# Performance work log

Hardware: AMD Instinct MI355X
Metric: run time of the kernel (lower is better)

The kernel has to match this reference:

```python
import jax, jax.numpy as jnp
import numpy as np
from jax import lax

EPS = 1e-5

def _odconv(x, W, fc_w, bn_g, bn_b, ch_w, ch_b, fl_w, fl_b, sp_w, sp_b, kn_w, kn_b):
    # x: [B,Cin,H,W]; W: [K,Cout,Cin,ks,ks] (kernel_num K candidate kernels)
    B = x.shape[0]
    K, Cout, Cin, ks, _ = W.shape
    pooled = jnp.mean(x, (2, 3))                          # global avg pool -> [B,Cin]
    h = pooled @ fc_w.T                                   # 1x1 conv (no bias) -> [B,A]
    m = jnp.mean(h, 0)
    v = jnp.var(h, 0)
    h = jax.nn.relu((h - m) * lax.rsqrt(v + EPS) * bn_g + bn_b)  # BN (train mode, batch stats)
    ch_att = jax.nn.sigmoid(h @ ch_w.T + ch_b)            # channel attention [B,Cin]
    fl_att = jax.nn.sigmoid(h @ fl_w.T + fl_b)            # filter attention  [B,Cout]
    sp_att = jax.nn.sigmoid(h @ sp_w.T + sp_b).reshape(B, 1, 1, 1, ks, ks)   # spatial
    kn_att = jax.nn.softmax(h @ kn_w.T + kn_b, axis=1).reshape(B, K, 1, 1, 1, 1)  # kernel
    # per-sample aggregated kernel: sum_k kn_att*sp_att*W -> [B,Cout,Cin,ks,ks]
    agg_w = jnp.sum(kn_att * sp_att * W[None], axis=1)
    xw = x * ch_att[:, :, None, None]
    pad = (ks - 1) // 2
    def conv1(xi, wi):  # per-sample conv == batch-as-groups trick in torch
        return lax.conv_general_dilated(xi[None], wi, (1, 1), [(pad, pad), (pad, pad)],
                                        dimension_numbers=('NCHW', 'OIHW', 'NCHW'))[0]
    out = jax.vmap(conv1)(xw, agg_w)                      # [B,Cout,H,W]
    return out * fl_att[:, :, None, None]

def _bn_relu(x, g, b):
    m = jnp.mean(x, (0, 2, 3), keepdims=True)
    v = jnp.var(x, (0, 2, 3), keepdims=True)
    return jax.nn.relu((x - m) * lax.rsqrt(v + EPS) * g.reshape(1, -1, 1, 1) + b.reshape(1, -1, 1, 1))

def setup_inputs() -> dict:
    key = jax.random.key(0)
    B, Cin, Cout, H, Wd = 16, 64, 128, 128, 128
    K, ks, A = 4, 3, 16  # kernel_num, kernel_size, attention_channel=max(int(C*0.0625),16)
    ks_ = [jax.random.fold_in(key, i) for i in range(32)]
    n = lambda k, shp, s=0.05: jax.random.normal(k, shp, jnp.float32) * s
    d = {'x': jax.random.normal(ks_[0], (B, Cin, H, Wd), jnp.float32)}
    # layer 1 (Cin->Cout)
    d.update(w1=n(ks_[1], (K, Cout, Cin, ks, ks)),
             a_fc_w=n(ks_[2], (A, Cin)), a_bn_g=jnp.ones(A), a_bn_b=jnp.zeros(A),
             a_ch_w=n(ks_[3], (Cin, A)), a_ch_b=jnp.zeros(Cin),
             a_fl_w=n(ks_[4], (Cout, A)), a_fl_b=jnp.zeros(Cout),
             a_sp_w=n(ks_[5], (ks * ks, A)), a_sp_b=jnp.zeros(ks * ks),
             a_kn_w=n(ks_[6], (K, A)), a_kn_b=jnp.zeros(K),
             bn1_g=jnp.ones(Cout), bn1_b=jnp.zeros(Cout))
    # layer 2 (Cout->Cout)
    d.update(w2=n(ks_[7], (K, Cout, Cout, ks, ks)),
             b_fc_w=n(ks_[8], (A, Cout)), b_bn_g=jnp.ones(A), b_bn_b=jnp.zeros(A),
             b_ch_w=n(ks_[9], (Cout, A)), b_ch_b=jnp.zeros(Cout),
             b_fl_w=n(ks_[10], (Cout, A)), b_fl_b=jnp.zeros(Cout),
             b_sp_w=n(ks_[11], (ks * ks, A)), b_sp_b=jnp.zeros(ks * ks),
             b_kn_w=n(ks_[12], (K, A)), b_kn_b=jnp.zeros(K),
             bn2_g=jnp.ones(Cout), bn2_b=jnp.zeros(Cout))
    return d

def reference(x, w1, a_fc_w, a_bn_g, a_bn_b, a_ch_w, a_ch_b, a_fl_w, a_fl_b,
              a_sp_w, a_sp_b, a_kn_w, a_kn_b, bn1_g, bn1_b,
              w2, b_fc_w, b_bn_g, b_bn_b, b_ch_w, b_ch_b, b_fl_w, b_fl_b,
              b_sp_w, b_sp_b, b_kn_w, b_kn_b, bn2_g, bn2_b):
    h = _odconv(x, w1, a_fc_w, a_bn_g, a_bn_b, a_ch_w, a_ch_b, a_fl_w, a_fl_b,
                a_sp_w, a_sp_b, a_kn_w, a_kn_b)
    h = _bn_relu(h, bn1_g, bn1_b)
    h = _odconv(h, w2, b_fc_w, b_bn_g, b_bn_b, b_ch_w, b_ch_b, b_fl_w, b_fl_b,
                b_sp_w, b_sp_b, b_kn_w, b_kn_b)
    return _bn_relu(h, bn2_g, bn2_b)
```

## Files before the change

### kernel.cpp

```cpp
#include <hip/hip_runtime.h>
#include <hip/hip_bf16.h>
#include <math.h>

#define EPS 1e-5f

typedef __attribute__((ext_vector_type(8))) short bf16x8;
typedef __attribute__((ext_vector_type(4))) float f32x4;

__device__ inline ushort f2bf(float f) {
    uint u = __float_as_uint(f);
    uint r = (u + 0x7fffu + ((u >> 16) & 1u)) >> 16;
    return (ushort)r;
}
__device__ inline float bf2f(ushort u) {
    return __uint_as_float(((uint)u) << 16);
}
__device__ inline float sigmoidf_(float x) { return 1.f / (1.f + expf(-x)); }

__device__ inline void gload16(const void* g, void* l) {
    __builtin_amdgcn_global_load_lds((const __attribute__((address_space(1))) unsigned int*)g,
                                     (__attribute__((address_space(3))) unsigned int*)l,
                                     16, 0, 0);
}

__global__ void attn_kernel(const float* __restrict__ pooled,
                            const float* __restrict__ fc_w,
                            const float* __restrict__ bn_g, const float* __restrict__ bn_b,
                            const float* __restrict__ ch_w, const float* __restrict__ ch_b,
                            const float* __restrict__ fl_w, const float* __restrict__ fl_b,
                            const float* __restrict__ sp_w, const float* __restrict__ sp_b,
                            const float* __restrict__ kn_w, const float* __restrict__ kn_b,
                            float* __restrict__ ch_att, float* __restrict__ fl_att,
                            float* __restrict__ sp_att, float* __restrict__ kn_att,
                            int C, int Cout) {
    const int Bb = 16, A = 16, K = 4;
    __shared__ float h[16][16];
    int tid = threadIdx.x;

    if (tid < Bb * A) {
        int b = tid >> 4, a = tid & 15;
        const float* pr = pooled + b * C;
        const float* fw = fc_w + a * C;
        float s = 0.f;
        for (int c = 0; c < C; c++) s += pr[c] * fw[c];
        h[b][a] = s;
    }
    __syncthreads();

    if (tid < A) {
        int a = tid;
        float m = 0.f;
        for (int b = 0; b < Bb; b++) m += h[b][a];
        m *= (1.f / 16.f);
        float v = 0.f;
        for (int b = 0; b < Bb; b++) { float d = h[b][a] - m; v += d * d; }
        v *= (1.f / 16.f);
        float inv = rsqrtf(v + EPS);
        float g = bn_g[a], bb = bn_b[a];
        for (int b = 0; b < Bb; b++) {
            float t = (h[b][a] - m) * inv * g + bb;
            h[b][a] = t > 0.f ? t : 0.f;
        }
    }
    __syncthreads();

    for (int idx = tid; idx < Bb * C; idx += blockDim.x) {
        int b = idx / C, c = idx % C;
        float s = ch_b[c];
        #pragma unroll
        for (int a = 0; a < A; a++) s += h[b][a] * ch_w[c * A + a];
        ch_att[idx] = sigmoidf_(s);
    }
    for (int idx = tid; idx < Bb * Cout; idx += blockDim.x) {
        int b = idx / Cout, o = idx % Cout;
        float s = fl_b[o];
        #pragma unroll
        for (int a = 0; a < A; a++) s += h[b][a] * fl_w[o * A + a];
        fl_att[idx] = sigmoidf_(s);
    }
    for (int idx = tid; idx < Bb * 9; idx += blockDim.x) {
        int b = idx / 9, r = idx % 9;
        float s = sp_b[r];
        #pragma unroll
        for (int a = 0; a < A; a++) s += h[b][a] * sp_w[r * A + a];
        sp_att[idx] = sigmoidf_(s);
    }
    if (tid < Bb) {
        int b = tid;
        float l[K], mx = -1e30f;
        #pragma unroll
        for (int k = 0; k < K; k++) {
            float s = kn_b[k];
            #pragma unroll
            for (int a = 0; a < A; a++) s += h[b][a] * kn_w[k * A + a];
            l[k] = s; mx = fmaxf(mx, s);
        }
        float den = 0.f;
        #pragma unroll
        for (int k = 0; k < K; k++) { l[k] = expf(l[k] - mx); den += l[k]; }
        #pragma unroll
        for (int k = 0; k < K; k++) kn_att[b * K + k] = l[k] / den;
    }
}

__global__ void waggF_kernel(const float* __restrict__ W4, const float* __restrict__ ch,
                             const float* __restrict__ fl, const float* __restrict__ sp,
                             const float* __restrict__ kn, ushort* __restrict__ WbF,
                             int Cout, int Cin, int NT, int N) {
    int idx = blockIdx.x * blockDim.x + threadIdx.x;
    if (idx >= N) return;
    int e = idx & 7;
    int l = (idx >> 3) & 63;
    int ot = (idx >> 9) & 7;
    int tb = idx >> 12;
    int t = tb % NT, b = tb / NT;
    int o = ot * 16 + (l & 15);
    int k = t * 32 + ((l >> 4) << 3) + e;
    int rs = k / Cin, i = k - rs * Cin;
    size_t kstride = (size_t)Cout * Cin * 9;
    const float* wp = W4 + ((size_t)o * Cin + i) * 9 + rs;
    const float* kp = kn + b * 4;
    float s = kp[0] * wp[0] + kp[1] * wp[kstride] + kp[2] * wp[2 * kstride] + kp[3] * wp[3 * kstride];
    float v = fl[b * Cout + o] * ch[b * Cin + i] * sp[b * 9 + rs] * s;
    WbF[idx] = f2bf(v);
}

__global__ __launch_bounds__(256) void trans_kernel(const float* __restrict__ in32,
                                                    const ushort* __restrict__ in16,
                                                    ushort* __restrict__ out,
                                                    float* __restrict__ ppart,
                                                    const float* __restrict__ stats,
                                                    const float* __restrict__ g,
                                                    const float* __restrict__ beta,
                                                    int C, int doBN) {
    int tilesC = C >> 5;
    int cbi = blockIdx.x % tilesC;
    int pbi = blockIdx.x / tilesC;
    int cb = cbi << 5, pb = pbi << 5;
    int y = blockIdx.y, b = blockIdx.z;
    __shared__ float tile[32][33];
    int t = threadIdx.x;
    int p = t & 31, c0 = t >> 5;
    float vj[4];
    #pragma unroll
    for (int j = 0; j < 4; j++) {
        int cl = c0 + j * 8;
        int c = cb + cl;
        size_t idx = (((size_t)b * C + c) * 128 + y) * 128 + pb + p;
        float v = in16 ? bf2f(in16[idx]) : in32[idx];
        if (doBN) {
            v = (v - stats[2 * c]) * stats[2 * c + 1] * g[c] + beta[c];
            v = fmaxf(v, 0.f);
        }
        tile[cl][p] = v;
        vj[j] = v;
    }
    #pragma unroll
    for (int j = 0; j < 4; j++) {
        float s = vj[j];
        #pragma unroll
        for (int msk = 1; msk < 32; msk <<= 1) s += __shfl_xor(s, msk);
        if (p == 0) {
            int cl = c0 + j * 8;
            ppart[((size_t)((b * tilesC + cbi) * 32 + cl)) * 512 + pbi * 128 + y] = s;
        }
    }
    __syncthreads();
    int c2 = (t & 15) << 1, pp = t >> 4;
    #pragma unroll
    for (int j = 0; j < 2; j++) {
        int p2 = pp + j * 16;
        uint lo = f2bf(tile[c2][p2]);
        uint hi = f2bf(tile[c2 + 1][p2]);
        *(uint*)&out[(((size_t)b * 128 + y) * 128 + pb + p2) * C + cb + c2] = lo | (hi << 16);
    }
}

__global__ void poolred_kernel(const float* __restrict__ part, float* __restrict__ pool) {
    int bc = blockIdx.x;
    const float* p = part + (size_t)bc * 512;
    float s = 0.f;
    for (int i = threadIdx.x; i < 512; i += 128) s += p[i];
    #pragma unroll
    for (int off = 32; off; off >>= 1) s += __shfl_down(s, off);
    __shared__ float tmp[2];
    if ((threadIdx.x & 63) == 0) tmp[threadIdx.x >> 6] = s;
    __syncthreads();
    if (!threadIdx.x) pool[bc] = (tmp[0] + tmp[1]) * (1.f / 16384.f);
}

__global__ __launch_bounds__(256, 3) void conv_mfma(const ushort* __restrict__ xT,
                                                    const ushort* __restrict__ WbF,
                                                    float* __restrict__ outF,
                                                    ushort* __restrict__ out16,
                                                    float* __restrict__ part,
                                                    int Cin, int use16) {
    const int BUFSH = 3 * 130 * 32;
    __shared__ short sx[2 * BUFSH];
    __shared__ float sred[4][64][2];
    int id = blockIdx.x;
    int swz = (id & 7) * (gridDim.x >> 3) + (id >> 3);
    int y = swz & 127, b = swz >> 7;
    int tid = threadIdx.x;
    int lane = tid & 63, wid = tid >> 6;
    int wm = wid >> 1, wn = wid & 1;
    int Cdiv32 = Cin >> 5;
    int NC = Cdiv32;
    int NT = 9 * Cdiv32;

    f32x4 acc[4][4] = {};

    {
        bf16x8 z = {};
        for (int e = tid * 8; e < 2 * BUFSH; e += 2048) *(bf16x8*)&sx[e] = z;
    }
    __syncthreads();

    const size_t rowstride = (size_t)128 * Cin;

    auto stage = [&](int bi, int ck) {
        #pragma unroll
        for (int j = 0; j < 6; j++) {
            int cc = wid + 4 * j;
            int r = cc >> 3, q = cc & 7;
            int yy = y + r - 1;
            if ((unsigned)yy < 128u) {
                int u = (q << 6) + lane;
                int P = (u >> 2) + 1;
                int slog = (u & 3) ^ ((P >> 1) & 3);
                const ushort* gp = xT + (size_t)(b * 128 + yy) * rowstride
                                      + (size_t)(P - 1) * Cin + (ck << 5) + (slog << 3);
                short* lp = &sx[bi * BUFSH + (r * 130 + 1) * 32 + (q << 9)];
                gload16(gp, lp);
            }
        }
    };

    stage(0, 0);
    __syncthreads();

    const bf16x8* Ab = (const bf16x8*)WbF;
    size_t abase = (size_t)b * NT;

    for (int ck = 0; ck < NC; ck++) {
        if (ck + 1 < NC) stage((ck + 1) & 1, ck + 1);
        const short* bb = &sx[(ck & 1) * BUFSH];
        #pragma unroll
        for (int rs = 0; rs < 9; rs++) {
            int rr = (rs / 3) * 130;
            int dx = rs % 3 - 1;
            int t = rs * Cdiv32 + ck;
            bf16x8 a[4], bv[4];
            size_t ai = ((abase + t) * 8 + wm * 4) * 64 + lane;
            #pragma unroll
            for (int m = 0; m < 4; m++) a[m] = Ab[ai + (size_t)m * 64];
            int Pb = wn * 64 + (lane & 15) + dx + 1;
            int slog = lane >> 4;
            #pragma unroll
            for (int n = 0; n < 4; n++) {
                int P = Pb + n * 16;
                bv[n] = *(const bf16x8*)&bb[(rr + P) * 32 + ((slog ^ ((P >> 1) & 3)) << 3)];
            }
            #pragma unroll
            for (int m = 0; m < 4; m++)
                #pragma unroll
                for (int n = 0; n < 4; n++)
                    acc[m][n] = __builtin_amdgcn_mfma_f32_16x16x32_bf16(
                        a[m], bv[n], acc[m][n], 0, 0, 0);
        }
        __syncthreads();
    }

    int px = wn * 64 + (lane & 15);
    int orow0 = wm * 64 + ((lane >> 4) << 2);
    if (use16) {
        #pragma unroll
        for (int m = 0; m < 4; m++)
            #pragma unroll
            for (int r = 0; r < 4; r++) {
                int oc = orow0 + m * 16 + r;
                ushort* po = out16 + ((size_t)(b * 128 + oc) * 128 + y) * 128 + px;
                #pragma unroll
                for (int n = 0; n < 4; n++) po[n * 16] = f2bf(acc[m][n][r]);
            }
    } else {
        #pragma unroll
        for (int m = 0; m < 4; m++)
            #pragma unroll
            for (int r = 0; r < 4; r++) {
                int oc = orow0 + m * 16 + r;
                float* po = outF + ((size_t)(b * 128 + oc) * 128 + y) * 128 + px;
                #pragma unroll
                for (int n = 0; n < 4; n++) po[n * 16] = acc[m][n][r];
            }
    }

    #pragma unroll
    for (int m = 0; m < 4; m++)
        #pragma unroll
        for (int r = 0; r < 4; r++) {
            float s = 0.f, q = 0.f;
            #pragma unroll
            for (int n = 0; n < 4; n++) { float v = acc[m][n][r]; s += v; q += v * v; }
            #pragma unroll
            for (int msk = 1; msk < 16; msk <<= 1) {
                s += __shfl_xor(s, msk);
                q += __shfl_xor(q, msk);
            }
            if ((lane & 15) == 0) {
                int chl = m * 16 + ((lane >> 4) << 2) + r;
                sred[wid][chl][0] = s;
                sred[wid][chl][1] = q;
            }
        }
    __syncthreads();
    {
        int ch = tid >> 1, v = tid & 1;
        int wmc = ch >> 6, chl = ch & 63;
        float t2 = sred[wmc * 2][chl][v] + sred[wmc * 2 + 1][chl][v];
        part[((size_t)(b * 128 + y)) * 256 + tid] = t2;
    }
}

__global__ void bnred_kernel(const float* __restrict__ part, float* __restrict__ stats) {
    int c = blockIdx.x;
    float s = 0.f, q = 0.f;
    for (int by = threadIdx.x; by < 2048; by += blockDim.x) {
        s += part[(size_t)by * 256 + 2 * c];
        q += part[(size_t)by * 256 + 2 * c + 1];
    }
    #pragma unroll
    for (int off = 32; off; off >>= 1) { s += __shfl_down(s, off); q += __shfl_down(q, off); }
    __shared__ float ss[4], qq[4];
    int lane = threadIdx.x & 63, w = threadIdx.x >> 6;
    if (!lane) { ss[w] = s; qq[w] = q; }
    __syncthreads();
    if (!threadIdx.x) {
        s = ss[0] + ss[1] + ss[2] + ss[3];
        q = qq[0] + qq[1] + qq[2] + qq[3];
        const float n = 16.f * 16384.f;
        float m = s / n;
        float var = q / n - m * m;
        stats[2 * c] = m;
        stats[2 * c + 1] = rsqrtf(var + EPS);
    }
}

__global__ void bnapply_kernel(float4* __restrict__ buf, const float* __restrict__ stats,
                               const float* __restrict__ g, const float* __restrict__ bta,
                               size_t N4) {
    size_t idx = (size_t)blockIdx.x * blockDim.x + threadIdx.x;
    size_t stride = (size_t)gridDim.x * blockDim.x;
    for (; idx < N4; idx += stride) {
        int c = (int)((idx >> 12) & 127);
        float sc = stats[2 * c + 1] * g[c];
        float sh = bta[c] - stats[2 * c] * sc;
        float4 v = buf[idx];
        v.x = fmaxf(v.x * sc + sh, 0.f);
        v.y = fmaxf(v.y * sc + sh, 0.f);
        v.z = fmaxf(v.z * sc + sh, 0.f);
        v.w = fmaxf(v.w * sc + sh, 0.f);
        buf[idx] = v;
    }
}

__global__ void bnapply16_kernel(const ushort* __restrict__ in, float4* __restrict__ out,
                                 const float* __restrict__ stats,
                                 const float* __restrict__ g, const float* __restrict__ bta,
                                 size_t N4) {
    size_t idx = (size_t)blockIdx.x * blockDim.x + threadIdx.x;
    size_t stride = (size_t)gridDim.x * blockDim.x;
    for (; idx < N4; idx += stride) {
        int c = (int)((idx >> 12) & 127);
        float sc = stats[2 * c + 1] * g[c];
        float sh = bta[c] - stats[2 * c] * sc;
        ushort4 u = *(const ushort4*)&in[idx * 4];
        float4 v;
        v.x = fmaxf(bf2f(u.x) * sc + sh, 0.f);
        v.y = fmaxf(bf2f(u.y) * sc + sh, 0.f);
        v.z = fmaxf(bf2f(u.z) * sc + sh, 0.f);
        v.w = fmaxf(bf2f(u.w) * sc + sh, 0.f);
        out[idx] = v;
    }
}

extern "C" void kernel_launch(void* const* d_in, const int* in_sizes, int n_in,
                              void* d_out, int out_size, void* d_ws, size_t ws_size,
                              hipStream_t stream) {
    const int B = 16, Cin1 = 64, C = 128, H = 128, W = 128, HW = H * W;

    const float* x      = (const float*)d_in[0];
    const float* w1     = (const float*)d_in[1];
    const float* a_fc_w = (const float*)d_in[2];
    const float* a_bn_g = (const float*)d_in[3];
    const float* a_bn_b = (const float*)d_in[4];
    const float* a_ch_w = (const float*)d_in[5];
    const float* a_ch_b = (const float*)d_in[6];
    const float* a_fl_w = (const float*)d_in[7];
    const float* a_fl_b = (const float*)d_in[8];
    const float* a_sp_w = (const float*)d_in[9];
    const float* a_sp_b = (const float*)d_in[10];
    const float* a_kn_w = (const float*)d_in[11];
    const float* a_kn_b = (const float*)d_in[12];
    const float* bn1_g  = (const float*)d_in[13];
    const float* bn1_b  = (const float*)d_in[14];
    const float* w2     = (const float*)d_in[15];
    const float* b_fc_w = (const float*)d_in[16];
    const float* b_bn_g = (const float*)d_in[17];
    const float* b_bn_b = (const float*)d_in[18];
    const float* b_ch_w = (const float*)d_in[19];
    const float* b_ch_b = (const float*)d_in[20];
    const float* b_fl_w = (const float*)d_in[21];
    const float* b_fl_b = (const float*)d_in[22];
    const float* b_sp_w = (const float*)d_in[23];
    const float* b_sp_b = (const float*)d_in[24];
    const float* b_kn_w = (const float*)d_in[25];
    const float* b_kn_b = (const float*)d_in[26];
    const float* bn2_g  = (const float*)d_in[27];
    const float* bn2_b  = (const float*)d_in[28];

    float* out = (float*)d_out;
    float* ws  = (float*)d_ws;

    float* XTf   = ws;
    ushort* xT   = (ushort*)XTf;
    float* WBf   = XTf + 16777216;
    ushort* WbF  = (ushort*)WBf;
    float* CPART = WBf + 1179648;
    float* PPART = CPART + 524288;
    float* POOL  = PPART + 1048576;
    float* CH    = POOL + 2048;
    float* FL    = CH + 2048;
    float* SP    = FL + 2048;
    float* KN    = SP + 160;
    float* ST    = KN + 64;
    float* XH2f  = ST + 256;
    ushort* xhat2 = (ushort*)XH2f;

    size_t need = ((size_t)(XH2f - ws) + 16777216) * sizeof(float);
    int fit2 = ws_size >= need;

    ushort* xhat1 = (ushort*)out;

    trans_kernel<<<dim3((Cin1 / 32) * 4, H, B), 256, 0, stream>>>(
        x, nullptr, xT, PPART, ST, nullptr, nullptr, Cin1, 0);
    poolred_kernel<<<B * Cin1, 128, 0, stream>>>(PPART, POOL);
    attn_kernel<<<1, 256, 0, stream>>>(POOL, a_fc_w, a_bn_g, a_bn_b, a_ch_w, a_ch_b,
                                       a_fl_w, a_fl_b, a_sp_w, a_sp_b, a_kn_w, a_kn_b,
                                       CH, FL, SP, KN, Cin1, C);
    int NT1 = 9 * Cin1 / 32;
    int N1 = B * NT1 * 4096;
    waggF_kernel<<<(N1 + 255) / 256, 256, 0, stream>>>(w1, CH, FL, SP, KN, WbF, C, Cin1, NT1, N1);
    conv_mfma<<<H * B, 256, 0, stream>>>(xT, WbF, nullptr, xhat1, CPART, Cin1, 1);
    bnred_kernel<<<C, 256, 0, stream>>>(CPART, ST);
    trans_kernel<<<dim3((C / 32) * 4, H, B), 256, 0, stream>>>(
        nullptr, xhat1, xT, PPART, ST, bn1_g, bn1_b, C, 1);

    poolred_kernel<<<B * C, 128, 0, stream>>>(PPART, POOL);
    attn_kernel<<<1, 256, 0, stream>>>(POOL, b_fc_w, b_bn_g, b_bn_b, b_ch_w, b_ch_b,
                                       b_fl_w, b_fl_b, b_sp_w, b_sp_b, b_kn_w, b_kn_b,
                                       CH, FL, SP, KN, C, C);
    int NT2 = 9 * C / 32;
    int N2 = B * NT2 * 4096;
    waggF_kernel<<<(N2 + 255) / 256, 256, 0, stream>>>(w2, CH, FL, SP, KN, WbF, C, C, NT2, N2);
    if (fit2) {
        conv_mfma<<<H * B, 256, 0, stream>>>(xT, WbF, nullptr, xhat2, CPART, C, 1);
        bnred_kernel<<<C, 256, 0, stream>>>(CPART, ST);
        bnapply16_kernel<<<2048, 256, 0, stream>>>(xhat2, (float4*)out, ST, bn2_g, bn2_b,
                                                   (size_t)B * C * HW / 4);
    } else {
        conv_mfma<<<H * B, 256, 0, stream>>>(xT, WbF, out, nullptr, CPART, C, 0);
        bnred_kernel<<<C, 256, 0, stream>>>(CPART, ST);
        bnapply_kernel<<<2048, 256, 0, stream>>>((float4*)out, ST, bn2_g, bn2_b,
                                                 (size_t)B * C * HW / 4);
    }
}
```

Measured before the change: 377.9 us.

## Compute two output rows per conv block to reuse staged input halo rows

The MFMA conv block now covers two output rows using 512 threads (8 waves), staging 4 input rows instead of 3 per row, so halo rows are shared between the two outputs. Per-output-row global/LDS staging traffic drops and weight (A) fragments are loaded per wave as before. The BN partial-sum reduction is restructured across 4 column/row waves, and bnred takes the new row count. LDS use grows and occupancy drops to 2 blocks of 512 threads, and the grid halves.

Measured after the change: 430.0 us. 1.14x slower.

```diff
diff --git a/kernel.cpp b/kernel.cpp
--- a/kernel.cpp
+++ b/kernel.cpp
@@ -189,21 +189,24 @@
     if (!threadIdx.x) pool[bc] = (tmp[0] + tmp[1]) * (1.f / 16384.f);
 }
 
-__global__ __launch_bounds__(256, 3) void conv_mfma(const ushort* __restrict__ xT,
+__global__ __launch_bounds__(512, 2) void conv_mfma(const ushort* __restrict__ xT,
                                                     const ushort* __restrict__ WbF,
                                                     float* __restrict__ outF,
                                                     ushort* __restrict__ out16,
                                                     float* __restrict__ part,
                                                     int Cin, int use16) {
-    const int BUFSH = 3 * 130 * 32;
+    const int BUFSH = 4 * 130 * 32;
     __shared__ short sx[2 * BUFSH];
-    __shared__ float sred[4][64][2];
+    __shared__ float sred[8][64][2];
     int id = blockIdx.x;
     int swz = (id & 7) * (gridDim.x >> 3) + (id >> 3);
-    int y = swz & 127, b = swz >> 7;
+    int yp = swz & 63, b = swz >> 6;
+    int y0 = yp << 1;
     int tid = threadIdx.x;
     int lane = tid & 63, wid = tid >> 6;
-    int wm = wid >> 1, wn = wid & 1;
+    int wm = wid >> 2;
+    int wn = wid & 3;
+    int wnrow = wn >> 1, wncol = wn & 1;
     int Cdiv32 = Cin >> 5;
     int NC = Cdiv32;
     int NT = 9 * Cdiv32;
@@ -212,7 +215,7 @@
 
     {
         bf16x8 z = {};
-        for (int e = tid * 8; e < 2 * BUFSH; e += 2048) *(bf16x8*)&sx[e] = z;
+        for (int e = tid * 8; e < 2 * BUFSH; e += 4096) *(bf16x8*)&sx[e] = z;
     }
     __syncthreads();
 
@@ -220,10 +223,10 @@
 
     auto stage = [&](int bi, int ck) {
         #pragma unroll
-        for (int j = 0; j < 6; j++) {
-            int cc = wid + 4 * j;
+        for (int j = 0; j < 4; j++) {
+            int cc = wid + 8 * j;
             int r = cc >> 3, q = cc & 7;
-            int yy = y + r - 1;
+            int yy = y0 + r - 1;
             if ((unsigned)yy < 128u) {
                 int u = (q << 6) + lane;
                 int P = (u >> 2) + 1;
@@ -247,19 +250,19 @@
         const short* bb = &sx[(ck & 1) * BUFSH];
         #pragma unroll
         for (int rs = 0; rs < 9; rs++) {
-            int rr = (rs / 3) * 130;
+            int rowL = wnrow + rs / 3;
             int dx = rs % 3 - 1;
             int t = rs * Cdiv32 + ck;
             bf16x8 a[4], bv[4];
             size_t ai = ((abase + t) * 8 + wm * 4) * 64 + lane;
             #pragma unroll
             for (int m = 0; m < 4; m++) a[m] = Ab[ai + (size_t)m * 64];
-            int Pb = wn * 64 + (lane & 15) + dx + 1;
+            int Pb = wncol * 64 + (lane & 15) + dx + 1;
             int slog = lane >> 4;
             #pragma unroll
             for (int n = 0; n < 4; n++) {
                 int P = Pb + n * 16;
-                bv[n] = *(const bf16x8*)&bb[(rr + P) * 32 + ((slog ^ ((P >> 1) & 3)) << 3)];
+                bv[n] = *(const bf16x8*)&bb[(rowL * 130 + P) * 32 + ((slog ^ ((P >> 1) & 3)) << 3)];
             }
             #pragma unroll
             for (int m = 0; m < 4; m++)
@@ -271,7 +274,8 @@
         __syncthreads();
     }
 
-    int px = wn * 64 + (lane & 15);
+    int y = y0 + wnrow;
+    int px = wncol * 64 + (lane & 15);
     int orow0 = wm * 64 + ((lane >> 4) << 2);
     if (use16) {
         #pragma unroll
@@ -309,23 +313,48 @@
             }
             if ((lane & 15) == 0) {
                 int chl = m * 16 + ((lane >> 4) << 2) + r;
-                sred[wid][chl][0] = s;
-                sred[wid][chl][1] = q;
+                if (wn == 0) { sred[wid][chl][0] = s; sred[wid][chl][1] = q; }
             }
         }
     __syncthreads();
-    {
+    #pragma unroll
+    for (int w2 = 1; w2 < 4; w2++) {
+        if (wn == w2) {
+            #pragma unroll
+            for (int m = 0; m < 4; m++)
+                #pragma unroll
+                for (int r = 0; r < 4; r++) {
+                    float s = 0.f, q = 0.f;
+                    #pragma unroll
+                    for (int n = 0; n < 4; n++) { float v = acc[m][n][r]; s += v; q += v * v; }
+                    #pragma unroll
+                    for (int msk = 1; msk < 16; msk <<= 1) {
+                        s += __shfl_xor(s, msk);
+                        q += __shfl_xor(q, msk);
+                    }
+                    if ((lane & 15) == 0) {
+                        int chl = m * 16 + ((lane >> 4) << 2) + r;
+                        sred[wm * 4 + w2][chl][0] = s;
+                        sred[wm * 4 + w2][chl][1] = q;
+                    }
+                }
+        }
+    }
+    __syncthreads();
+    if (tid < 256) {
         int ch = tid >> 1, v = tid & 1;
         int wmc = ch >> 6, chl = ch & 63;
-        float t2 = sred[wmc * 2][chl][v] + sred[wmc * 2 + 1][chl][v];
-        part[((size_t)(b * 128 + y)) * 256 + tid] = t2;
-    }
-}
-
-__global__ void bnred_kernel(const float* __restrict__ part, float* __restrict__ stats) {
+        float t2 = sred[wmc * 4 + 0][chl][v] + sred[wmc * 4 + 1][chl][v]
+                 + sred[wmc * 4 + 2][chl][v] + sred[wmc * 4 + 3][chl][v];
+        part[((size_t)(b * 64 + yp)) * 256 + tid] = t2;
+    }
+}
+
+__global__ void bnred_kernel(const float* __restrict__ part, float* __restrict__ stats,
+                             int nrows) {
     int c = blockIdx.x;
     float s = 0.f, q = 0.f;
-    for (int by = threadIdx.x; by < 2048; by += blockDim.x) {
+    for (int by = threadIdx.x; by < nrows; by += blockDim.x) {
         s += part[(size_t)by * 256 + 2 * c];
         q += part[(size_t)by * 256 + 2 * c + 1];
     }
@@ -451,8 +480,8 @@
     int NT1 = 9 * Cin1 / 32;
     int N1 = B * NT1 * 4096;
     waggF_kernel<<<(N1 + 255) / 256, 256, 0, stream>>>(w1, CH, FL, SP, KN, WbF, C, Cin1, NT1, N1);
-    conv_mfma<<<H * B, 256, 0, stream>>>(xT, WbF, nullptr, xhat1, CPART, Cin1, 1);
-    bnred_kernel<<<C, 256, 0, stream>>>(CPART, ST);
+    conv_mfma<<<H * B / 2, 512, 0, stream>>>(xT, WbF, nullptr, xhat1, CPART, Cin1, 1);
+    bnred_kernel<<<C, 256, 0, stream>>>(CPART, ST, 1024);
     trans_kernel<<<dim3((C / 32) * 4, H, B), 256, 0, stream>>>(
         nullptr, xhat1, xT, PPART, ST, bn1_g, bn1_b, C, 1);
 
@@ -464,13 +493,13 @@
     int N2 = B * NT2 * 4096;
     waggF_kernel<<<(N2 + 255) / 256, 256, 0, stream>>>(w2, CH, FL, SP, KN, WbF, C, C, NT2, N2);
     if (fit2) {
-        conv_mfma<<<H * B, 256, 0, stream>>>(xT, WbF, nullptr, xhat2, CPART, C, 1);
-        bnred_kernel<<<C, 256, 0, stream>>>(CPART, ST);
+        conv_mfma<<<H * B / 2, 512, 0, stream>>>(xT, WbF, nullptr, xhat2, CPART, C, 1);
+        bnred_kernel<<<C, 256, 0, stream>>>(CPART, ST, 1024);
         bnapply16_kernel<<<2048, 256, 0, stream>>>(xhat2, (float4*)out, ST, bn2_g, bn2_b,
                                                    (size_t)B * C * HW / 4);
     } else {
-        conv_mfma<<<H * B, 256, 0, stream>>>(xT, WbF, out, nullptr, CPART, C, 0);
-        bnred_kernel<<<C, 256, 0, stream>>>(CPART, ST);
+        conv_mfma<<<H * B / 2, 512, 0, stream>>>(xT, WbF, out, nullptr, CPART, C, 0);
+        bnred_kernel<<<C, 256, 0, stream>>>(CPART, ST, 1024);
         bnapply_kernel<<<2048, 256, 0, stream>>>((float4*)out, ST, bn2_g, bn2_b,
                                                  (size_t)B * C * HW / 4);
     }
```

## Switch conv to 32x32x16 MFMA with register-prefetched weights and templated Cin

Applied to the files above, without the earlier changes.

Replaces the 16x16x32 bf16 MFMA tiling with 32x32x16 MFMA fragments and re-lays out the aggregated weight buffer in 32-row by 16-k tiles to match. Weight fragments are now double-buffered in registers, with the next step's loads issued ahead of the current MFMAs. Cin becomes a template parameter so the loop over channel chunks and taps fully unrolls. The goals are fewer MFMA and LDS instructions per FLOP and hiding global weight-load latency, at the cost of more register pressure and a reworked epilogue and reduction mapping.

After: 417.5 us. 10.5% more time.

```diff
diff --git a/kernel.cpp b/kernel.cpp
--- a/kernel.cpp
+++ b/kernel.cpp
@@ -6,6 +6,7 @@
 
 typedef __attribute__((ext_vector_type(8))) short bf16x8;
 typedef __attribute__((ext_vector_type(4))) float f32x4;
+typedef __attribute__((ext_vector_type(16))) float f32x16;
 
 __device__ inline ushort f2bf(float f) {
     uint u = __float_as_uint(f);
@@ -106,17 +107,17 @@
 __global__ void waggF_kernel(const float* __restrict__ W4, const float* __restrict__ ch,
                              const float* __restrict__ fl, const float* __restrict__ sp,
                              const float* __restrict__ kn, ushort* __restrict__ WbF,
-                             int Cout, int Cin, int NT, int N) {
+                             int Cout, int Cin, int NK16, int NKT, int N) {
     int idx = blockIdx.x * blockDim.x + threadIdx.x;
     if (idx >= N) return;
     int e = idx & 7;
     int l = (idx >> 3) & 63;
-    int ot = (idx >> 9) & 7;
-    int tb = idx >> 12;
-    int t = tb % NT, b = tb / NT;
-    int o = ot * 16 + (l & 15);
-    int k = t * 32 + ((l >> 4) << 3) + e;
-    int rs = k / Cin, i = k - rs * Cin;
+    int ot = (idx >> 9) & 3;
+    int tb = idx >> 11;
+    int kt = tb % NKT, b = tb / NKT;
+    int o = (ot << 5) + (l & 31);
+    int rs = kt / NK16, i16 = kt - rs * NK16;
+    int i = (i16 << 4) + ((l >> 5) << 3) + e;
     size_t kstride = (size_t)Cout * Cin * 9;
     const float* wp = W4 + ((size_t)o * Cin + i) * 9 + rs;
     const float* kp = kn + b * 4;
@@ -189,26 +190,27 @@
     if (!threadIdx.x) pool[bc] = (tmp[0] + tmp[1]) * (1.f / 16384.f);
 }
 
+template<int CIN>
 __global__ __launch_bounds__(256, 3) void conv_mfma(const ushort* __restrict__ xT,
                                                     const ushort* __restrict__ WbF,
                                                     float* __restrict__ outF,
                                                     ushort* __restrict__ out16,
                                                     float* __restrict__ part,
-                                                    int Cin, int use16) {
+                                                    int use16) {
     const int BUFSH = 3 * 130 * 32;
     __shared__ short sx[2 * BUFSH];
     __shared__ float sred[4][64][2];
+    const int NK16 = CIN >> 4;
+    const int NC = CIN >> 5;
+    const int NKT = 9 * NK16;
     int id = blockIdx.x;
     int swz = (id & 7) * (gridDim.x >> 3) + (id >> 3);
     int y = swz & 127, b = swz >> 7;
     int tid = threadIdx.x;
     int lane = tid & 63, wid = tid >> 6;
     int wm = wid >> 1, wn = wid & 1;
-    int Cdiv32 = Cin >> 5;
-    int NC = Cdiv32;
-    int NT = 9 * Cdiv32;
-
-    f32x4 acc[4][4] = {};
+
+    f32x16 acc[2][2] = {};
 
     {
         bf16x8 z = {};
@@ -216,7 +218,7 @@
     }
     __syncthreads();
 
-    const size_t rowstride = (size_t)128 * Cin;
+    const size_t rowstride = (size_t)128 * CIN;
 
     auto stage = [&](int bi, int ck) {
         #pragma unroll
@@ -229,7 +231,7 @@
                 int P = (u >> 2) + 1;
                 int slog = (u & 3) ^ ((P >> 1) & 3);
                 const ushort* gp = xT + (size_t)(b * 128 + yy) * rowstride
-                                      + (size_t)(P - 1) * Cin + (ck << 5) + (slog << 3);
+                                      + (size_t)(P - 1) * CIN + (ck << 5) + (slog << 3);
                 short* lp = &sx[bi * BUFSH + (r * 130 + 1) * 32 + (q << 9)];
                 gload16(gp, lp);
             }
@@ -237,78 +239,90 @@
     };
 
     stage(0, 0);
-    __syncthreads();
 
     const bf16x8* Ab = (const bf16x8*)WbF;
-    size_t abase = (size_t)b * NT;
-
-    for (int ck = 0; ck < NC; ck++) {
-        if (ck + 1 < NC) stage((ck + 1) & 1, ck + 1);
+    const size_t abase = (size_t)b * NKT;
+
+    bf16x8 aR[2][2][2];
+    #pragma unroll
+    for (int kt2 = 0; kt2 < 2; kt2++)
+        #pragma unroll
+        for (int mf = 0; mf < 2; mf++)
+            aR[0][kt2][mf] = Ab[((abase + kt2) * 4 + (wm * 2 + mf)) * 64 + lane];
+
+    __syncthreads();
+
+    int pxb = wn * 64 + (lane & 31);
+    int sb = lane >> 5;
+
+    #pragma unroll
+    for (int s = 0; s < NC * 9; s++) {
+        const int ck = s / 9, rs = s % 9, cur = s & 1;
+        if (rs == 0 && ck + 1 < NC) stage((ck + 1) & 1, ck + 1);
+        if (s + 1 < NC * 9) {
+            const int ck1 = (s + 1) / 9, rs1 = (s + 1) % 9;
+            const int kt0 = rs1 * NK16 + ck1 * 2;
+            #pragma unroll
+            for (int kt2 = 0; kt2 < 2; kt2++)
+                #pragma unroll
+                for (int mf = 0; mf < 2; mf++)
+                    aR[cur ^ 1][kt2][mf] =
+                        Ab[((abase + kt0 + kt2) * 4 + (wm * 2 + mf)) * 64 + lane];
+        }
         const short* bb = &sx[(ck & 1) * BUFSH];
-        #pragma unroll
-        for (int rs = 0; rs < 9; rs++) {
-            int rr = (rs / 3) * 130;
-            int dx = rs % 3 - 1;
-            int t = rs * Cdiv32 + ck;
-            bf16x8 a[4], bv[4];
-            size_t ai = ((abase + t) * 8 + wm * 4) * 64 + lane;
+        const int rr = (rs / 3) * 130;
+        const int dx = rs % 3 - 1;
+        bf16x8 bv[2][2];
+        #pragma unroll
+        for (int kt2 = 0; kt2 < 2; kt2++)
             #pragma unroll
-            for (int m = 0; m < 4; m++) a[m] = Ab[ai + (size_t)m * 64];
-            int Pb = wn * 64 + (lane & 15) + dx + 1;
-            int slog = lane >> 4;
+            for (int nf = 0; nf < 2; nf++) {
+                int P = pxb + nf * 32 + dx + 1;
+                int slot = ((kt2 << 1) + sb) ^ ((P >> 1) & 3);
+                bv[kt2][nf] = *(const bf16x8*)&bb[(rr + P) * 32 + (slot << 3)];
+            }
+        #pragma unroll
+        for (int kt2 = 0; kt2 < 2; kt2++)
             #pragma unroll
-            for (int n = 0; n < 4; n++) {
-                int P = Pb + n * 16;
-                bv[n] = *(const bf16x8*)&bb[(rr + P) * 32 + ((slog ^ ((P >> 1) & 3)) << 3)];
+            for (int mf = 0; mf < 2; mf++)
+                #pragma unroll
+                for (int nf = 0; nf < 2; nf++)
+                    acc[mf][nf] = __builtin_amdgcn_mfma_f32_32x32x16_bf16(
+                        aR[cur][kt2][mf], bv[kt2][nf], acc[mf][nf], 0, 0, 0);
+        if (rs == 8 && ck + 1 < NC) __syncthreads();
+    }
+
+    int pxs = wn * 64 + (lane & 31);
+    #pragma unroll
+    for (int mf = 0; mf < 2; mf++)
+        #pragma unroll
+        for (int reg = 0; reg < 16; reg++) {
+            int oc = wm * 64 + mf * 32 + (reg & 3) + ((reg >> 2) << 3) + ((lane >> 5) << 2);
+            if (use16) {
+                ushort* po = out16 + ((size_t)(b * 128 + oc) * 128 + y) * 128 + pxs;
+                po[0]  = f2bf(acc[mf][0][reg]);
+                po[32] = f2bf(acc[mf][1][reg]);
+            } else {
+                float* po = outF + ((size_t)(b * 128 + oc) * 128 + y) * 128 + pxs;
+                po[0]  = acc[mf][0][reg];
+                po[32] = acc[mf][1][reg];
             }
+        }
+
+    #pragma unroll
+    for (int mf = 0; mf < 2; mf++)
+        #pragma unroll
+        for (int reg = 0; reg < 16; reg++) {
+            float v0 = acc[mf][0][reg], v1 = acc[mf][1][reg];
+            float s = v0 + v1;
+            float q = v0 * v0 + v1 * v1;
             #pragma unroll
-            for (int m = 0; m < 4; m++)
-                #pragma unroll
-                for (int n = 0; n < 4; n++)
-                    acc[m][n] = __builtin_amdgcn_mfma_f32_16x16x32_bf16(
-                        a[m], bv[n], acc[m][n], 0, 0, 0);
-        }
-        __syncthreads();
-    }
-
-    int px = wn * 64 + (lane & 15);
-    int orow0 = wm * 64 + ((lane >> 4) << 2);
-    if (use16) {
-        #pragma unroll
-        for (int m = 0; m < 4; m++)
-            #pragma unroll
-            for (int r = 0; r < 4; r++) {
-                int oc = orow0 + m * 16 + r;
-                ushort* po = out16 + ((size_t)(b * 128 + oc) * 128 + y) * 128 + px;
-                #pragma unroll
-                for (int n = 0; n < 4; n++) po[n * 16] = f2bf(acc[m][n][r]);
-            }
-    } else {
-        #pragma unroll
-        for (int m = 0; m < 4; m++)
-            #pragma unroll
-            for (int r = 0; r < 4; r++) {
-                int oc = orow0 + m * 16 + r;
-                float* po = outF + ((size_t)(b * 128 + oc) * 128 + y) * 128 + px;
-                #pragma unroll
-                for (int n = 0; n < 4; n++) po[n * 16] = acc[m][n][r];
-            }
-    }
-
-    #pragma unroll
-    for (int m = 0; m < 4; m++)
-        #pragma unroll
-        for (int r = 0; r < 4; r++) {
-            float s = 0.f, q = 0.f;
-            #pragma unroll
-            for (int n = 0; n < 4; n++) { float v = acc[m][n][r]; s += v; q += v * v; }
-            #pragma unroll
-            for (int msk = 1; msk < 16; msk <<= 1) {
+            for (int msk = 1; msk < 32; msk <<= 1) {
                 s += __shfl_xor(s, msk);
                 q += __shfl_xor(q, msk);
             }
-            if ((lane & 15) == 0) {
-                int chl = m * 16 + ((lane >> 4) << 2) + r;
+            if ((lane & 31) == 0) {
+                int chl = mf * 32 + (reg & 3) + ((reg >> 2) << 3) + ((lane >> 5) << 2);
                 sred[wid][chl][0] = s;
                 sred[wid][chl][1] = q;
             }
@@ -322,10 +336,11 @@
     }
 }
 
-__global__ void bnred_kernel(const float* __restrict__ part, float* __restrict__ stats) {
+__global__ void bnred_kernel(const float* __restrict__ part, float* __restrict__ stats,
+                             int nrows) {
     int c = blockIdx.x;
     float s = 0.f, q = 0.f;
-    for (int by = threadIdx.x; by < 2048; by += blockDim.x) {
+    for (int by = threadIdx.x; by < nrows; by += blockDim.x) {
         s += part[(size_t)by * 256 + 2 * c];
         q += part[(size_t)by * 256 + 2 * c + 1];
     }
@@ -448,11 +463,12 @@
     attn_kernel<<<1, 256, 0, stream>>>(POOL, a_fc_w, a_bn_g, a_bn_b, a_ch_w, a_ch_b,
                                        a_fl_w, a_fl_b, a_sp_w, a_sp_b, a_kn_w, a_kn_b,
                                        CH, FL, SP, KN, Cin1, C);
-    int NT1 = 9 * Cin1 / 32;
-    int N1 = B * NT1 * 4096;
-    waggF_kernel<<<(N1 + 255) / 256, 256, 0, stream>>>(w1, CH, FL, SP, KN, WbF, C, Cin1, NT1, N1);
-    conv_mfma<<<H * B, 256, 0, stream>>>(xT, WbF, nullptr, xhat1, CPART, Cin1, 1);
-    bnred_kernel<<<C, 256, 0, stream>>>(CPART, ST);
+    int NK16_1 = Cin1 / 16, NKT1 = 9 * NK16_1;
+    int N1 = B * NKT1 * 2048;
+    waggF_kernel<<<(N1 + 255) / 256, 256, 0, stream>>>(w1, CH, FL, SP, KN, WbF, C, Cin1,
+                                                       NK16_1, NKT1, N1);
+    conv_mfma<64><<<H * B, 256, 0, stream>>>(xT, WbF, nullptr, xhat1, CPART, 1);
+    bnred_kernel<<<C, 256, 0, stream>>>(CPART, ST, 2048);
     trans_kernel<<<dim3((C / 32) * 4, H, B), 256, 0, stream>>>(
         nullptr, xhat1, xT, PPART, ST, bn1_g, bn1_b, C, 1);
 
@@ -460,17 +476,18 @@
     attn_kernel<<<1, 256, 0, stream>>>(POOL, b_fc_w, b_bn_g, b_bn_b, b_ch_w, b_ch_b,
                                        b_fl_w, b_fl_b, b_sp_w, b_sp_b, b_kn_w, b_kn_b,
                                        CH, FL, SP, KN, C, C);
-    int NT2 = 9 * C / 32;
-    int N2 = B * NT2 * 4096;
-    waggF_kernel<<<(N2 + 255) / 256, 256, 0, stream>>>(w2, CH, FL, SP, KN, WbF, C, C, NT2, N2);
+    int NK16_2 = C / 16, NKT2 = 9 * NK16_2;
+    int N2 = B * NKT2 * 2048;
+    waggF_kernel<<<(N2 + 255) / 256, 256, 0, stream>>>(w2, CH, FL, SP, KN, WbF, C, C,
+                                                       NK16_2, NKT2, N2);
     if (fit2) {
-        conv_mfma<<<H * B, 256, 0, stream>>>(xT, WbF, nullptr, xhat2, CPART, C, 1);
-        bnred_kernel<<<C, 256, 0, stream>>>(CPART, ST);
+        conv_mfma<128><<<H * B, 256, 0, stream>>>(xT, WbF, nullptr, xhat2, CPART, 1);
+        bnred_kernel<<<C, 256, 0, stream>>>(CPART, ST, 2048);
         bnapply16_kernel<<<2048, 256, 0, stream>>>(xhat2, (float4*)out, ST, bn2_g, bn2_b,
                                                    (size_t)B * C * HW / 4);
     } else {
-        conv_mfma<<<H * B, 256, 0, stream>>>(xT, WbF, out, nullptr, CPART, C, 0);
-        bnred_kernel<<<C, 256, 0, stream>>>(CPART, ST);
+        conv_mfma<128><<<H * B, 256, 0, stream>>>(xT, WbF, out, nullptr, CPART, 0);
+        bnred_kernel<<<C, 256, 0, stream>>>(CPART, ST, 2048);
         bnapply_kernel<<<2048, 256, 0, stream>>>((float4*)out, ST, bn2_g, bn2_b,
                                                  (size_t)B * C * HW / 4);
     }
```
